# Performance work log

Measured on AMD Instinct MI355X. Metric: run time of the kernel, lower is better.

The kernel has to match this reference:

```python
import jax, jax.numpy as jnp
import numpy as np

HASH = 1 << 12
EPS = 1e-5
_OFFS = [(dx, dy, dz) for dx in (-1, 0, 1) for dy in (-1, 0, 1) for dz in (-1, 0, 1)]
_KOFF = [k for k, o in enumerate(_OFFS) if o != (0, 0, 0)]  # 26 non-center taps
_CENTER = 13


def _hkey(c):
    c = c.astype(np.int64)
    return (c[:, 0] * HASH + c[:, 1]) * HASH + c[:, 2]


def _rand_coords(rng, n, R):
    idx = rng.choice(R ** 3, size=n, replace=False)
    return np.stack(np.unravel_index(idx, (R, R, R)), axis=1).astype(np.int64)


def _conv3_maps(coords):
    # ME kernel map for a 3x3x3 stride-1 conv (in coords == out coords):
    # per non-center tap, (gather_idx, scatter_idx) pairs found by hash lookup.
    n = coords.shape[0]
    keys = _hkey(coords)
    order = np.argsort(keys)
    skeys = keys[order]
    ins, outs = [], []
    for k in _KOFF:
        qk = _hkey(coords + np.asarray(_OFFS[k], np.int64))
        pos = np.clip(np.searchsorted(skeys, qk), 0, n - 1)
        valid = skeys[pos] == qk
        outs.append(np.nonzero(valid)[0].astype(np.int32))
        ins.append(order[pos[valid]].astype(np.int32))
    m = max(len(a) for a in ins)
    im = np.zeros((26, m), np.int32)    # pad gathers with row 0
    om = np.full((26, m), n, np.int32)  # pad scatters into scrap row n (dropped)
    for j in range(26):
        im[j, :len(ins[j])] = ins[j]
        om[j, :len(outs[j])] = outs[j]
    return np.stack([im, om])  # [2, 26, M]


def _children(coords):
    # generative transpose conv k=2 s=2 output coords, ordered o*n + i
    offs = np.array([[a, b, c] for a in (0, 1) for b in (0, 1) for c in (0, 1)], np.int64)
    return (2 * coords[None] + offs[:, None]).reshape(-1, 3)


def _union(ca, cb):
    # sparse-tensor addition domain: union of coordinate sets
    ka, kb = _hkey(ca), _hkey(cb)
    ku = np.unique(np.concatenate([ka, kb]))
    cu = np.stack([ku // (HASH * HASH), (ku // HASH) % HASH, ku % HASH], axis=1)
    return cu, np.searchsorted(ku, ka).astype(np.int32), np.searchsorted(ku, kb).astype(np.int32)


def _sconv3(x, W, m):
    # sparse 3^3 conv as gather-GEMM-scatter; center tap is a plain GEMM
    n = x.shape[0]
    acc = jnp.zeros((n + 1, W.shape[2]), x.dtype)
    for j, k in enumerate(_KOFF):
        acc = acc.at[m[1, j]].add(x[m[0, j]] @ W[k])
    return acc[:n] + x @ W[_CENTER]


def _bn_elu(x, p):
    # MinkowskiBatchNorm (training-mode batch stats over active voxels) + ELU
    mu = jnp.mean(x, axis=0)
    var = jnp.mean(jnp.square(x - mu), axis=0)
    return jax.nn.elu(p[0] * (x - mu) * jax.lax.rsqrt(var + EPS) + p[1])


def _up_block(x, Wt, Wc, m, pa, pb):
    # generative transpose conv (every voxel emits 8 children, order o*n+i) -> BN -> ELU -> conv3 -> BN -> ELU
    t = jnp.einsum('nc,ocd->ond', x, Wt).reshape(-1, Wt.shape[2])
    return _bn_elu(_sconv3(_bn_elu(t, pa), Wc, m), pb)


def setup_inputs() -> dict:
    rng = np.random.default_rng(0)
    N2, N1, N0 = 1200, 6000, 16000
    C2 = _rand_coords(rng, N2, 40)
    C1 = _rand_coords(rng, N1, 80)
    C0 = _rand_coords(rng, N0, 160)
    G2 = _children(C2)                       # coords after up_block_2 transpose conv
    U1, lat1_idx, up1_idx = _union(C1, G2)   # inputs[1] + x domain
    G1 = _children(U1)
    U0, lat0_idx, up0_idx = _union(C0, G1)   # inputs[0] + x domain

    key = jax.random.key(0)
    ks = list(jax.random.split(key, 32))
    kit = iter(ks)

    def w(shape, fan_in):
        return jax.random.normal(next(kit), shape, jnp.float32) * np.float32(1.0 / np.sqrt(fan_in))

    def bn(c):
        g = 1.0 + 0.1 * jax.random.normal(next(kit), (c,), jnp.float32)
        b = 0.1 * jax.random.normal(next(kit), (c,), jnp.float32)
        return jnp.stack([g, b])

    return dict(
        feats0=jax.random.normal(next(kit), (N0, 64), jnp.float32),
        feats1=jax.random.normal(next(kit), (N1, 128), jnp.float32),
        feats2=jax.random.normal(next(kit), (N2, 256), jnp.float32),
        w_out0=w((27, 64, 128), 27 * 64),
        w_out1=w((27, 128, 128), 27 * 128),
        w_out2=w((27, 256, 128), 27 * 256),
        wt2=w((8, 256, 128), 256),
        wu2=w((27, 128, 128), 27 * 128),
        wt1=w((8, 128, 64), 128),
        wu1=w((27, 64, 64), 27 * 64),
        bn_out0=bn(128), bn_out1=bn(128), bn_out2=bn(128),
        bn_up2a=bn(128), bn_up2b=bn(128),
        bn_up1a=bn(64), bn_up1b=bn(64),
        u1_base=jnp.zeros((U1.shape[0], 128), jnp.float32),
        u0_base=jnp.zeros((U0.shape[0], 64), jnp.float32),
        m_c2=jnp.asarray(_conv3_maps(C2)),
        m_g2=jnp.asarray(_conv3_maps(G2)),
        m_u1=jnp.asarray(_conv3_maps(U1)),
        m_g1=jnp.asarray(_conv3_maps(G1)),
        m_u0=jnp.asarray(_conv3_maps(U0)),
        lat1_idx=jnp.asarray(lat1_idx), up1_idx=jnp.asarray(up1_idx),
        lat0_idx=jnp.asarray(lat0_idx), up0_idx=jnp.asarray(up0_idx),
    )


def reference(feats0, feats1, feats2, w_out0, w_out1, w_out2, wt2, wu2, wt1, wu1,
              bn_out0, bn_out1, bn_out2, bn_up2a, bn_up2b, bn_up1a, bn_up1b,
              u1_base, u0_base, m_c2, m_g2, m_u1, m_g1, m_u0,
              lat1_idx, up1_idx, lat0_idx, up0_idx):
    # i = 2 (top)
    out2 = _bn_elu(_sconv3(feats2, w_out2, m_c2), bn_out2)
    t = _up_block(feats2, wt2, wu2, m_g2, bn_up2a, bn_up2b)
    # i = 1: sparse add over union of coords, then out/up blocks
    x1 = u1_base.at[lat1_idx].add(feats1).at[up1_idx].add(t)
    out1 = _bn_elu(_sconv3(x1, w_out1, m_u1), bn_out1)
    t = _up_block(x1, wt1, wu1, m_g1, bn_up1a, bn_up1b)
    # i = 0
    x0 = u0_base.at[lat0_idx].add(feats0).at[up0_idx].add(t)
    out0 = _bn_elu(_sconv3(x0, w_out0, m_u0), bn_out0)
    return out0, out1, out2
```

## Files before the change

### kernel.cpp

```cpp
#include <hip/hip_runtime.h>

typedef __bf16 bf16x8 __attribute__((ext_vector_type(8)));
typedef float  f32x4  __attribute__((ext_vector_type(4)));
typedef unsigned short u16x8 __attribute__((ext_vector_type(8)));

__device__ __forceinline__ float b2f(unsigned short u) {
    union { unsigned int i; float f; } v; v.i = ((unsigned int)u) << 16; return v.f;
}
__device__ __forceinline__ unsigned short f2b(float f) {
    union { float f; unsigned int i; } v; v.f = f;
    unsigned int u = v.i;
    return (unsigned short)((u + 0x7fffu + ((u >> 16) & 1u)) >> 16);
}

__global__ void table_init(int* __restrict__ tab, int n)
{
    int idx = blockIdx.x * blockDim.x + threadIdx.x;
    if (idx >= n * 27) return;
    tab[idx] = ((idx % 27) == 13) ? (idx / 27) : n;
}

__global__ void table_fill(int* __restrict__ tab, const int* __restrict__ map, int M, int n)
{
    int tid = blockIdx.x * blockDim.x + threadIdx.x;
    if (tid >= 26 * M) return;
    int j = tid / M, q = tid - j * M;
    int om = map[(26 + j) * M + q];
    if (om < n) {
        int k = (j < 13) ? j : j + 1;
        tab[om * 27 + k] = map[j * M + q];
    }
}

__global__ void pack_w(const float* __restrict__ W, unsigned short* __restrict__ P,
                       int total, int log2Cout, int log2KC)
{
    int tid = blockIdx.x * blockDim.x + threadIdx.x;
    if (tid >= total) return;
    int jj   = tid & 7;
    int cout = (tid >> 3) & ((1 << log2Cout) - 1);
    int rest = tid >> (3 + log2Cout);
    int quad = rest & 3;
    int kj   = rest >> 2;
    int kc   = kj & ((1 << log2KC) - 1);
    int j    = kj >> log2KC;
    int Cin  = (1 << log2KC) * 32;
    int Cout = 1 << log2Cout;
    P[tid] = f2b(W[((size_t)j * Cin + kc * 32 + quad * 8 + jj) * Cout + cout]);
}

__global__ void cast_bf16(const float* __restrict__ X, unsigned short* __restrict__ Y, int nElem)
{
    int tid = blockIdx.x * blockDim.x + threadIdx.x;
    if (tid < nElem) Y[tid] = f2b(X[tid]);
}

template<int T, int KC, int RT, bool OUTBF16>
__global__ __launch_bounds__(256) void conv_mfma_st(
    const unsigned short* __restrict__ Xb, const unsigned short* __restrict__ P,
    const int* __restrict__ tab, void* __restrict__ OutV, float* __restrict__ St,
    int n, int nblk)
{
    constexpr int Cin = KC * 32, Cout = 64 * T;
    constexpr int ROWS = RT * 16;
    constexpr int STRIDE = KC * 32 + 8;
    constexpr int CHUNKS = KC * 4;
    constexpr int RPR = 256 / CHUNKS;
    constexpr int NRD = ROWS / RPR;
    __shared__ int tps[ROWS * 27];
    __shared__ unsigned short abuf[2][ROWS * STRIDE];

    const int t = threadIdx.x, lane = t & 63, wv = t >> 6;
    const int m = lane & 15, quad = lane >> 4;

    const int q = nblk >> 3, rr = nblk & 7;
    const int xcd = blockIdx.x & 7, pos = blockIdx.x >> 3;
    const int bswz = (xcd < rr) ? (xcd * (q + 1) + pos) : (rr * (q + 1) + (xcd - rr) * q + pos);
    const int r0 = bswz * ROWS;
    int rows = n - r0; if (rows > ROWS) rows = ROWS;

    for (int e = t; e < ROWS * 27; e += 256)
        tps[e] = (e < rows * 27) ? tab[(size_t)r0 * 27 + e] : n;
    __syncthreads();

    const int sr = t / CHUNKS;
    const int sc = t % CHUNKS;

    f32x4 acc[RT][T];
    #pragma unroll
    for (int rt = 0; rt < RT; rt++)
        #pragma unroll
        for (int c = 0; c < T; c++) acc[rt][c] = f32x4{0.f, 0.f, 0.f, 0.f};

    uint4 sreg[NRD];

    #pragma unroll
    for (int rd = 0; rd < NRD; rd++) {
        int r = rd * RPR + sr;
        int in = tps[r * 27];
        sreg[rd] = *reinterpret_cast<const uint4*>(Xb + (size_t)in * Cin + sc * 8);
    }
    #pragma unroll
    for (int rd = 0; rd < NRD; rd++) {
        int r = rd * RPR + sr;
        *reinterpret_cast<uint4*>(&abuf[0][r * STRIDE + sc * 8]) = sreg[rd];
    }
    __syncthreads();

    for (int j = 0; j < 27; j++) {
        const int cur = j & 1;
        if (j + 1 < 27) {
            #pragma unroll
            for (int rd = 0; rd < NRD; rd++) {
                int r = rd * RPR + sr;
                int in = tps[r * 27 + j + 1];
                sreg[rd] = *reinterpret_cast<const uint4*>(Xb + (size_t)in * Cin + sc * 8);
            }
        }
        #pragma unroll
        for (int kc = 0; kc < KC; kc++) {
            bf16x8 a[RT];
            #pragma unroll
            for (int rt = 0; rt < RT; rt++)
                a[rt] = *reinterpret_cast<const bf16x8*>(&abuf[cur][(rt * 16 + m) * STRIDE + kc * 32 + quad * 8]);
            const unsigned short* bp = P + ((size_t)((j * KC + kc) * 4 + quad) * Cout + wv * (T * 16)) * 8;
            #pragma unroll
            for (int c = 0; c < T; c++) {
                bf16x8 b = *reinterpret_cast<const bf16x8*>(bp + (c * 16 + m) * 8);
                #pragma unroll
                for (int rt = 0; rt < RT; rt++)
                    acc[rt][c] = __builtin_amdgcn_mfma_f32_16x16x32_bf16(a[rt], b, acc[rt][c], 0, 0, 0);
            }
        }
        if (j + 1 < 27) {
            #pragma unroll
            for (int rd = 0; rd < NRD; rd++) {
                int r = rd * RPR + sr;
                *reinterpret_cast<uint4*>(&abuf[cur ^ 1][r * STRIDE + sc * 8]) = sreg[rd];
            }
        }
        __syncthreads();
    }

    #pragma unroll
    for (int c = 0; c < T; c++) {
        const int cout = (wv * T + c) * 16 + m;
        float s = 0.f, ss = 0.f;
        #pragma unroll
        for (int rt = 0; rt < RT; rt++) {
            #pragma unroll
            for (int reg = 0; reg < 4; reg++) {
                int r = rt * 16 + quad * 4 + reg;
                if (r < rows) {
                    float v = acc[rt][c][reg];
                    size_t off = (size_t)(r0 + r) * Cout + cout;
                    if (OUTBF16) {
                        unsigned short h = f2b(v);
                        ((unsigned short*)OutV)[off] = h;
                        v = b2f(h);
                    } else {
                        ((float*)OutV)[off] = v;
                    }
                    s += v; ss += v * v;
                }
            }
        }
        if (St) {
            s  += __shfl_xor(s, 16);  ss += __shfl_xor(ss, 16);
            s  += __shfl_xor(s, 32);  ss += __shfl_xor(ss, 32);
            if (quad == 0) {
                float* Sr = St + (size_t)(blockIdx.x & 7) * 2 * Cout;
                atomicAdd(&Sr[cout], s);
                atomicAdd(&Sr[Cout + cout], ss);
            }
        }
    }
}

template<int T, int RB, bool OUTBF16>
__global__ __launch_bounds__(256) void conv_mfma(
    const unsigned short* __restrict__ Xb, const unsigned short* __restrict__ P,
    const int* __restrict__ tab, void* __restrict__ OutV, int n, int Cin, int KC, int nblk)
{
    const int Cout = 64 * T;
    const int ROWS = RB * 16;
    __shared__ int tps[RB * 16 * 27];
    __shared__ int vld[27];
    const int t = threadIdx.x, lane = t & 63, wv = t >> 6;
    const int m = lane & 15, quad = lane >> 4;

    const int q = nblk >> 3, rr = nblk & 7;
    const int xcd = blockIdx.x & 7, pos = blockIdx.x >> 3;
    const int bswz = (xcd < rr) ? (xcd * (q + 1) + pos) : (rr * (q + 1) + (xcd - rr) * q + pos);
    const int r0 = bswz * ROWS;
    int rows = n - r0; if (rows > ROWS) rows = ROWS;

    for (int e = t; e < ROWS * 27; e += 256)
        tps[e] = (e < rows * 27) ? tab[(size_t)r0 * 27 + e] : n;
    __syncthreads();
    if constexpr (RB == 1) {
        if (t < 27) {
            int v = 0;
            for (int r = 0; r < 16; r++) v |= (tps[r * 27 + t] < n) ? 1 : 0;
            vld[t] = v;
        }
        __syncthreads();
    }

    f32x4 acc[RB][T];
    #pragma unroll
    for (int rt = 0; rt < RB; rt++)
        #pragma unroll
        for (int c = 0; c < T; c++) acc[rt][c] = f32x4{0.f, 0.f, 0.f, 0.f};

    const unsigned short* Xq = Xb + quad * 8;
    const unsigned short* Pq = P + ((size_t)quad * Cout + wv * (T * 16)) * 8;

    for (int j = 0; j < 27; j++) {
        if constexpr (RB == 1) {
            if (!vld[j]) continue;
        }
        int in[RB];
        #pragma unroll
        for (int rt = 0; rt < RB; rt++) in[rt] = tps[(rt * 16 + m) * 27 + j];
        for (int kc = 0; kc < KC; kc++) {
            bf16x8 a[RB];
            #pragma unroll
            for (int rt = 0; rt < RB; rt++)
                a[rt] = *reinterpret_cast<const bf16x8*>(Xq + (size_t)in[rt] * Cin + kc * 32);
            const unsigned short* bp = Pq + (size_t)((j * KC + kc) * 4) * Cout * 8;
            #pragma unroll
            for (int c = 0; c < T; c++) {
                bf16x8 b = *reinterpret_cast<const bf16x8*>(bp + (c * 16 + m) * 8);
                #pragma unroll
                for (int rt = 0; rt < RB; rt++)
                    acc[rt][c] = __builtin_amdgcn_mfma_f32_16x16x32_bf16(a[rt], b, acc[rt][c], 0, 0, 0);
            }
        }
    }

    #pragma unroll
    for (int c = 0; c < T; c++) {
        int cout = (wv * T + c) * 16 + m;
        #pragma unroll
        for (int rt = 0; rt < RB; rt++) {
            #pragma unroll
            for (int reg = 0; reg < 4; reg++) {
                int r = rt * 16 + quad * 4 + reg;
                if (r < rows) {
                    size_t off = (size_t)(r0 + r) * Cout + cout;
                    if (OUTBF16) ((unsigned short*)OutV)[off] = f2b(acc[rt][c][reg]);
                    else         ((float*)OutV)[off] = acc[rt][c][reg];
                }
            }
        }
    }
}

template<int KC, int T>
__global__ __launch_bounds__(256) void tconv_mfma(
    const unsigned short* __restrict__ Xb, const unsigned short* __restrict__ P,
    unsigned short* __restrict__ Out, int n)
{
    const int Cin = KC * 32, Cout = 64 * T;
    const int t = threadIdx.x, lane = t & 63, wv = t >> 6;
    const int m = lane & 15, quad = lane >> 4;
    const int r0 = blockIdx.x * 16;
    int rows = n - r0; if (rows > 16) rows = 16;

    bf16x8 a[KC];
    #pragma unroll
    for (int kc = 0; kc < KC; kc++) {
        a[kc] = bf16x8{};
        if (m < rows)
            a[kc] = *reinterpret_cast<const bf16x8*>(Xb + (size_t)(r0 + m) * Cin + kc * 32 + quad * 8);
    }

    for (int o = 0; o < 8; o++) {
        f32x4 acc[T];
        #pragma unroll
        for (int c = 0; c < T; c++) acc[c] = f32x4{0.f, 0.f, 0.f, 0.f};
        #pragma unroll
        for (int kc = 0; kc < KC; kc++) {
            const unsigned short* bp = P + ((size_t)((o * KC + kc) * 4 + quad) * Cout + wv * (T * 16)) * 8;
            #pragma unroll
            for (int c = 0; c < T; c++) {
                bf16x8 b = *reinterpret_cast<const bf16x8*>(bp + (c * 16 + m) * 8);
                acc[c] = __builtin_amdgcn_mfma_f32_16x16x32_bf16(a[kc], b, acc[c], 0, 0, 0);
            }
        }
        #pragma unroll
        for (int c = 0; c < T; c++) {
            int cout = (wv * T + c) * 16 + m;
            #pragma unroll
            for (int reg = 0; reg < 4; reg++) {
                int r = quad * 4 + reg;
                if (r < rows)
                    Out[((size_t)o * n + r0 + r) * Cout + cout] = f2b(acc[c][reg]);
            }
        }
    }
}

__global__ void scatter_add_f32(float* __restrict__ dst, const float* __restrict__ src,
                                const int* __restrict__ idx, long total, int C)
{
    long tid = (long)blockIdx.x * blockDim.x + threadIdx.x;
    if (tid >= total) return;
    long r = tid / C;
    int  c = (int)(tid - r * C);
    dst[(long)idx[r] * C + c] += src[tid];
}

__global__ void scatter_add_b16(float* __restrict__ dst, const unsigned short* __restrict__ src,
                                const int* __restrict__ idx, long total, int C)
{
    long tid = (long)blockIdx.x * blockDim.x + threadIdx.x;
    if (tid >= total) return;
    long r = tid / C;
    int  c = (int)(tid - r * C);
    dst[(long)idx[r] * C + c] += b2f(src[tid]);
}

template<bool BF16>
__global__ void bn_stats_k(const void* __restrict__ Xv, float* __restrict__ stats,
                           int n, int C, int rowsPerBlock)
{
    const int t = threadIdx.x;
    const int c = t & (C - 1);
    const int sub = t / C;
    const int nsub = 256 / C;
    int r0 = blockIdx.x * rowsPerBlock + sub;
    int r1 = blockIdx.x * rowsPerBlock + rowsPerBlock;
    if (r1 > n) r1 = n;
    float s = 0.f, ss = 0.f;
    for (int r = r0; r < r1; r += nsub) {
        float v = BF16 ? b2f(((const unsigned short*)Xv)[(long)r * C + c])
                       : ((const float*)Xv)[(long)r * C + c];
        s += v; ss += v * v;
    }
    __shared__ float bs[256];
    __shared__ float bq[256];
    bs[t] = s; bq[t] = ss;
    __syncthreads();
    if (sub == 0) {
        for (int k = 1; k < nsub; k++) { s += bs[k * C + c]; ss += bq[k * C + c]; }
        atomicAdd(&stats[c], s);
        atomicAdd(&stats[C + c], ss);
    }
}

__global__ void bn_finalize(const float* __restrict__ stats, const float* __restrict__ gb,
                            float* __restrict__ scsh, int C, float invn, int nrep)
{
    int c = threadIdx.x;
    if (c >= C) return;
    float sm = 0.f, sq = 0.f;
    for (int r = 0; r < nrep; r++) {
        sm += stats[r * 2 * C + c];
        sq += stats[r * 2 * C + C + c];
    }
    float mu  = sm * invn;
    float var = sq * invn - mu * mu;
    float sc  = gb[c] * rsqrtf(var + 1e-5f);
    scsh[c]     = sc;
    scsh[C + c] = gb[C + c] - mu * sc;
}

__global__ void bn_apply_f32v(float* __restrict__ X, const float* __restrict__ scsh,
                              long total4, int C)
{
    long tid = (long)blockIdx.x * blockDim.x + threadIdx.x;
    if (tid >= total4) return;
    int c0 = (int)((tid * 4) & (C - 1));
    float4 x  = reinterpret_cast<float4*>(X)[tid];
    float4 sc = *reinterpret_cast<const float4*>(&scsh[c0]);
    float4 sh = *reinterpret_cast<const float4*>(&scsh[C + c0]);
    float v0 = x.x * sc.x + sh.x; v0 = (v0 > 0.f) ? v0 : expm1f(v0);
    float v1 = x.y * sc.y + sh.y; v1 = (v1 > 0.f) ? v1 : expm1f(v1);
    float v2 = x.z * sc.z + sh.z; v2 = (v2 > 0.f) ? v2 : expm1f(v2);
    float v3 = x.w * sc.w + sh.w; v3 = (v3 > 0.f) ? v3 : expm1f(v3);
    reinterpret_cast<float4*>(X)[tid] = float4{v0, v1, v2, v3};
}

__global__ void bn_apply_b16v(unsigned short* __restrict__ X, const float* __restrict__ scsh,
                              long total8, int C)
{
    long tid = (long)blockIdx.x * blockDim.x + threadIdx.x;
    if (tid >= total8) return;
    int c0 = (int)((tid * 8) & (C - 1));
    u16x8 x = reinterpret_cast<u16x8*>(X)[tid];
    u16x8 y;
    #pragma unroll
    for (int k = 0; k < 8; k++) {
        float v = b2f(x[k]) * scsh[c0 + k] + scsh[C + c0 + k];
        v = (v > 0.f) ? v : expm1f(v);
        y[k] = f2b(v);
    }
    reinterpret_cast<u16x8*>(X)[tid] = y;
}

extern "C" void kernel_launch(void* const* d_in, const int* in_sizes, int n_in,
                              void* d_out, int out_size, void* d_ws, size_t ws_size,
                              hipStream_t stream)
{
    const float* feats0  = (const float*)d_in[0];
    const float* feats1  = (const float*)d_in[1];
    const float* feats2  = (const float*)d_in[2];
    const float* w_out0  = (const float*)d_in[3];
    const float* w_out1  = (const float*)d_in[4];
    const float* w_out2  = (const float*)d_in[5];
    const float* wt2     = (const float*)d_in[6];
    const float* wu2     = (const float*)d_in[7];
    const float* wt1     = (const float*)d_in[8];
    const float* wu1     = (const float*)d_in[9];
    const float* bn_out0 = (const float*)d_in[10];
    const float* bn_out1 = (const float*)d_in[11];
    const float* bn_out2 = (const float*)d_in[12];
    const float* bn_up2a = (const float*)d_in[13];
    const float* bn_up2b = (const float*)d_in[14];
    const float* bn_up1a = (const float*)d_in[15];
    const float* bn_up1b = (const float*)d_in[16];
    const int* m_c2 = (const int*)d_in[19];
    const int* m_g2 = (const int*)d_in[20];
    const int* m_u1 = (const int*)d_in[21];
    const int* m_g1 = (const int*)d_in[22];
    const int* m_u0 = (const int*)d_in[23];
    const int* lat1 = (const int*)d_in[24];
    const int* up1  = (const int*)d_in[25];
    const int* lat0 = (const int*)d_in[26];
    const int* up0  = (const int*)d_in[27];

    const int N0  = in_sizes[0] / 64;
    const int N1  = in_sizes[1] / 128;
    const int N2  = in_sizes[2] / 256;
    const int U1  = in_sizes[17] / 128;
    const int U0  = in_sizes[18] / 64;
    const int G2n = in_sizes[25];
    const int G1n = in_sizes[27];
    const int Mc2 = in_sizes[19] / 52;
    const int Mg2 = in_sizes[20] / 52;
    const int Mu1 = in_sizes[21] / 52;
    const int Mg1 = in_sizes[22] / 52;
    const int Mu0 = in_sizes[23] / 52;

    float* out0 = (float*)d_out;
    float* out1 = out0 + (size_t)U0 * 128;
    float* out2 = out1 + (size_t)U1 * 128;

    char* wp = (char*)d_ws;
    auto alloc = [&](size_t bytes) -> char* {
        char* r = wp; wp += (bytes + 255) & ~(size_t)255; return r;
    };
    float*          x0   = (float*)alloc((size_t)U0 * 64 * 4);
    unsigned short* t1   = (unsigned short*)alloc((size_t)(G1n + 1) * 64 * 2);
    unsigned short* t1c  = (unsigned short*)alloc((size_t)(G1n + 1) * 64 * 2);
    unsigned short* t2   = (unsigned short*)alloc((size_t)(G2n + 1) * 128 * 2);
    unsigned short* t2c  = (unsigned short*)alloc((size_t)(G2n + 1) * 128 * 2);
    float*          x1   = (float*)alloc((size_t)U1 * 128 * 4);
    unsigned short* x1b  = (unsigned short*)alloc((size_t)(U1 + 1) * 128 * 2);
    unsigned short* x0b  = (unsigned short*)alloc((size_t)(U0 + 1) * 64 * 2);
    unsigned short* f2bb = (unsigned short*)alloc((size_t)(N2 + 1) * 256 * 2);
    unsigned short* pc2  = (unsigned short*)alloc((size_t)27 * 256 * 128 * 2);
    unsigned short* pt2  = (unsigned short*)alloc((size_t)8  * 256 * 128 * 2);
    unsigned short* pg2  = (unsigned short*)alloc((size_t)27 * 128 * 128 * 2);
    unsigned short* pu1  = (unsigned short*)alloc((size_t)27 * 128 * 128 * 2);
    unsigned short* pt1  = (unsigned short*)alloc((size_t)8  * 128 * 64  * 2);
    unsigned short* pg1  = (unsigned short*)alloc((size_t)27 * 64  * 64  * 2);
    unsigned short* pu0  = (unsigned short*)alloc((size_t)27 * 64  * 128 * 2);
    int maxSmall = (U1 > G2n) ? U1 : G2n;
    int*   smallTab = (int*)alloc((size_t)maxSmall * 27 * 4);
    float* stats    = (float*)alloc(8 * 2 * 128 * 4);
    float* scsh     = (float*)alloc(2 * 128 * 4);
    int* tab_g1 = (int*)x0;
    int* tab_u0 = (int*)t1;

    hipMemsetAsync(f2bb + (size_t)N2  * 256, 0, 256 * 2, stream);
    hipMemsetAsync(t2   + (size_t)G2n * 128, 0, 128 * 2, stream);
    hipMemsetAsync(x1b  + (size_t)U1  * 128, 0, 128 * 2, stream);
    hipMemsetAsync(t1   + (size_t)G1n * 64,  0, 64  * 2, stream);
    hipMemsetAsync(x0b  + (size_t)U0  * 64,  0, 64  * 2, stream);

    auto packW = [&](const float* W, unsigned short* P, int taps, int l2co, int l2kc) {
        int total = taps * ((1 << l2kc) * 32) * (1 << l2co);
        pack_w<<<dim3((total + 255) / 256), dim3(256), 0, stream>>>(W, P, total, l2co, l2kc);
    };
    auto cast = [&](const float* X, unsigned short* Y, long nElem) {
        cast_bf16<<<dim3((int)((nElem + 255) / 256)), dim3(256), 0, stream>>>(X, Y, (int)nElem);
    };
    auto buildTab = [&](int* tab, const int* map, int M, int n) {
        table_init<<<dim3((n * 27 + 255) / 256), dim3(256), 0, stream>>>(tab, n);
        table_fill<<<dim3((26 * M + 255) / 256), dim3(256), 0, stream>>>(tab, map, M, n);
    };
    auto conv = [&](const unsigned short* Xb, const unsigned short* P, const int* tab,
                    void* Out, int n, int Cin, int Cout, bool outbf16, float* st) {
        int KC = Cin / 32;
        if (n >= 12000) {
            if (Cout == 128 && KC == 2) {
                int nblk = (n + 63) / 64;
                dim3 g(nblk), b(256);
                if (outbf16) conv_mfma_st<2, 2, 4, true ><<<g, b, 0, stream>>>(Xb, P, tab, Out, st, n, nblk);
                else         conv_mfma_st<2, 2, 4, false><<<g, b, 0, stream>>>(Xb, P, tab, Out, st, n, nblk);
                return;
            }
            if (Cout == 64 && KC == 2) {
                int nblk = (n + 63) / 64;
                dim3 g(nblk), b(256);
                if (outbf16) conv_mfma_st<1, 2, 4, true ><<<g, b, 0, stream>>>(Xb, P, tab, Out, st, n, nblk);
                else         conv_mfma_st<1, 2, 4, false><<<g, b, 0, stream>>>(Xb, P, tab, Out, st, n, nblk);
                return;
            }
            if (Cout == 128 && KC == 4) {
                int nblk = (n + 31) / 32;
                dim3 g(nblk), b(256);
                if (outbf16) conv_mfma_st<2, 4, 2, true ><<<g, b, 0, stream>>>(Xb, P, tab, Out, st, n, nblk);
                else         conv_mfma_st<2, 4, 2, false><<<g, b, 0, stream>>>(Xb, P, tab, Out, st, n, nblk);
                return;
            }
        }
        int RB = (n >= 12000) ? 2 : 1;
        int nblk = (n + RB * 16 - 1) / (RB * 16);
        dim3 g(nblk), b(256);
        #define CONV_CASE(T_, RB_)                                                                        \
            if (Cout == 64 * T_ && RB == RB_) {                                                           \
                if (outbf16) conv_mfma<T_, RB_, true ><<<g, b, 0, stream>>>(Xb, P, tab, Out, n, Cin, KC, nblk); \
                else         conv_mfma<T_, RB_, false><<<g, b, 0, stream>>>(Xb, P, tab, Out, n, Cin, KC, nblk); \
                return;                                                                                   \
            }
        CONV_CASE(2, 2) CONV_CASE(2, 1)
        CONV_CASE(1, 2) CONV_CASE(1, 1)
        #undef CONV_CASE
    };
    auto bnapply = [&](void* X, const float* gb, int n, int C, bool bf16, int nrep) {
        bn_finalize<<<dim3(1), dim3(C), 0, stream>>>(stats, gb, scsh, C, 1.0f / n, nrep);
        if (bf16) {
            long tot8 = (long)n * C / 8;
            bn_apply_b16v<<<dim3((int)((tot8 + 255) / 256)), dim3(256), 0, stream>>>((unsigned short*)X, scsh, tot8, C);
        } else {
            long tot4 = (long)n * C / 4;
            bn_apply_f32v<<<dim3((int)((tot4 + 255) / 256)), dim3(256), 0, stream>>>((float*)X, scsh, tot4, C);
        }
    };
    auto bnelu = [&](void* X, const float* gb, int n, int C, bool bf16) {
        hipMemsetAsync(stats, 0, 2 * C * sizeof(float), stream);
        const int rpb = 512;
        if (bf16) bn_stats_k<true ><<<dim3((n + rpb - 1) / rpb), dim3(256), 0, stream>>>(X, stats, n, C, rpb);
        else      bn_stats_k<false><<<dim3((n + rpb - 1) / rpb), dim3(256), 0, stream>>>(X, stats, n, C, rpb);
        bnapply(X, gb, n, C, bf16, 1);
    };

    cast(feats2, f2bb, (long)N2 * 256);
    packW(w_out2, pc2, 27, 7, 3);
    packW(wt2,    pt2,  8, 7, 3);
    packW(wu2,    pg2, 27, 7, 2);
    packW(w_out1, pu1, 27, 7, 2);
    packW(wt1,    pt1,  8, 6, 2);
    packW(wu1,    pg1, 27, 6, 1);
    packW(w_out0, pu0, 27, 7, 1);

    buildTab(smallTab, m_c2, Mc2, N2);
    conv(f2bb, pc2, smallTab, out2, N2, 256, 128, false, nullptr);
    bnelu(out2, bn_out2, N2, 128, false);
    tconv_mfma<8, 2><<<dim3((N2 + 15) / 16), dim3(256), 0, stream>>>(f2bb, pt2, t2, N2);
    bnelu(t2, bn_up2a, G2n, 128, true);
    buildTab(smallTab, m_g2, Mg2, G2n);
    conv(t2, pg2, smallTab, t2c, G2n, 128, 128, true, nullptr);
    bnelu(t2c, bn_up2b, G2n, 128, true);

    hipMemsetAsync(x1, 0, (size_t)U1 * 128 * sizeof(float), stream);
    {
        long tot = (long)N1 * 128;
        scatter_add_f32<<<dim3((int)((tot + 255) / 256)), dim3(256), 0, stream>>>(x1, feats1, lat1, tot, 128);
        tot = (long)G2n * 128;
        scatter_add_b16<<<dim3((int)((tot + 255) / 256)), dim3(256), 0, stream>>>(x1, t2c, up1, tot, 128);
    }
    cast(x1, x1b, (long)U1 * 128);
    buildTab(smallTab, m_u1, Mu1, U1);
    hipMemsetAsync(stats, 0, 8 * 2 * 128 * sizeof(float), stream);
    conv(x1b, pu1, smallTab, out1, U1, 128, 128, false, stats);
    bnapply(out1, bn_out1, U1, 128, false, 8);
    tconv_mfma<4, 1><<<dim3((U1 + 15) / 16), dim3(256), 0, stream>>>(x1b, pt1, t1, U1);
    bnelu(t1, bn_up1a, G1n, 64, true);
    buildTab(tab_g1, m_g1, Mg1, G1n);
    hipMemsetAsync(stats, 0, 8 * 2 * 64 * sizeof(float), stream);
    conv(t1, pg1, tab_g1, t1c, G1n, 64, 64, true, stats);
    bnapply(t1c, bn_up1b, G1n, 64, true, 8);

    hipMemsetAsync(x0, 0, (size_t)U0 * 64 * sizeof(float), stream);
    {
        long tot = (long)N0 * 64;
        scatter_add_f32<<<dim3((int)((tot + 255) / 256)), dim3(256), 0, stream>>>(x0, feats0, lat0, tot, 64);
        tot = (long)G1n * 64;
        scatter_add_b16<<<dim3((int)((tot + 255) / 256)), dim3(256), 0, stream>>>(x0, t1c, up0, tot, 64);
    }
    buildTab(tab_u0, m_u0, Mu0, U0);
    cast(x0, x0b, (long)U0 * 64);
    hipMemsetAsync(stats, 0, 8 * 2 * 128 * sizeof(float), stream);
    conv(x0b, pu0, tab_u0, out0, U0, 64, 128, false, stats);
    bnapply(out0, bn_out0, U0, 128, false, 8);
}
```

Baseline: 950.1 us.

## Fuse BN+ELU into scatter-add, vectorize cast/scatter kernels, enlarge conv row tile

```diff
diff --git a/kernel.cpp b/kernel.cpp
--- a/kernel.cpp
+++ b/kernel.cpp
@@ -49,10 +49,13 @@
     P[tid] = f2b(W[((size_t)j * Cin + kc * 32 + quad * 8 + jj) * Cout + cout]);
 }
 
-__global__ void cast_bf16(const float* __restrict__ X, unsigned short* __restrict__ Y, int nElem)
-{
-    int tid = blockIdx.x * blockDim.x + threadIdx.x;
-    if (tid < nElem) Y[tid] = f2b(X[tid]);
+__global__ void cast_bf16v(const float* __restrict__ X, unsigned short* __restrict__ Y, long total4)
+{
+    long tid = (long)blockIdx.x * blockDim.x + threadIdx.x;
+    if (tid >= total4) return;
+    float4 x = reinterpret_cast<const float4*>(X)[tid];
+    ushort4 y{f2b(x.x), f2b(x.y), f2b(x.z), f2b(x.w)};
+    reinterpret_cast<ushort4*>(Y)[tid] = y;
 }
 
 template<int T, int KC, int RT, bool OUTBF16>
@@ -302,24 +305,40 @@
     }
 }
 
-__global__ void scatter_add_f32(float* __restrict__ dst, const float* __restrict__ src,
-                                const int* __restrict__ idx, long total, int C)
+__global__ void scatter_set_f32v(float* __restrict__ dst, const float* __restrict__ src,
+                                 const int* __restrict__ idx, long total4, int C4)
 {
     long tid = (long)blockIdx.x * blockDim.x + threadIdx.x;
-    if (tid >= total) return;
-    long r = tid / C;
-    int  c = (int)(tid - r * C);
-    dst[(long)idx[r] * C + c] += src[tid];
-}
-
-__global__ void scatter_add_b16(float* __restrict__ dst, const unsigned short* __restrict__ src,
-                                const int* __restrict__ idx, long total, int C)
+    if (tid >= total4) return;
+    long r = tid / C4;
+    int  c4 = (int)(tid - r * C4);
+    float4 s = reinterpret_cast<const float4*>(src)[tid];
+    reinterpret_cast<float4*>(dst + (long)idx[r] * C4 * 4)[c4] = s;
+}
+
+__global__ void scatter_bn_add_b16v(float* __restrict__ dst, const unsigned short* __restrict__ src,
+                                    const int* __restrict__ idx, const float* __restrict__ scsh,
+                                    long total8, int C)
 {
     long tid = (long)blockIdx.x * blockDim.x + threadIdx.x;
-    if (tid >= total) return;
-    long r = tid / C;
-    int  c = (int)(tid - r * C);
-    dst[(long)idx[r] * C + c] += b2f(src[tid]);
+    if (tid >= total8) return;
+    int C8 = C >> 3;
+    long r = tid / C8;
+    int  c0 = (int)(tid - r * C8) * 8;
+    u16x8 x = reinterpret_cast<const u16x8*>(src)[tid];
+    float* d = dst + (long)idx[r] * C + c0;
+    float4 d0 = *reinterpret_cast<float4*>(d);
+    float4 d1 = *reinterpret_cast<float4*>(d + 4);
+    float v[8];
+    #pragma unroll
+    for (int k = 0; k < 8; k++) {
+        float w = b2f(x[k]) * scsh[c0 + k] + scsh[C + c0 + k];
+        v[k] = (w > 0.f) ? w : expm1f(w);
+    }
+    d0.x += v[0]; d0.y += v[1]; d0.z += v[2]; d0.w += v[3];
+    d1.x += v[4]; d1.y += v[5]; d1.z += v[6]; d1.w += v[7];
+    *reinterpret_cast<float4*>(d)     = d0;
+    *reinterpret_cast<float4*>(d + 4) = d1;
 }
 
 template<bool BF16>
@@ -486,7 +505,8 @@
         pack_w<<<dim3((total + 255) / 256), dim3(256), 0, stream>>>(W, P, total, l2co, l2kc);
     };
     auto cast = [&](const float* X, unsigned short* Y, long nElem) {
-        cast_bf16<<<dim3((int)((nElem + 255) / 256)), dim3(256), 0, stream>>>(X, Y, (int)nElem);
+        long tot4 = nElem / 4;
+        cast_bf16v<<<dim3((int)((tot4 + 255) / 256)), dim3(256), 0, stream>>>(X, Y, tot4);
     };
     auto buildTab = [&](int* tab, const int* map, int M, int n) {
         table_init<<<dim3((n * 27 + 255) / 256), dim3(256), 0, stream>>>(tab, n);
@@ -504,10 +524,10 @@
                 return;
             }
             if (Cout == 64 && KC == 2) {
-                int nblk = (n + 63) / 64;
+                int nblk = (n + 127) / 128;
                 dim3 g(nblk), b(256);
-                if (outbf16) conv_mfma_st<1, 2, 4, true ><<<g, b, 0, stream>>>(Xb, P, tab, Out, st, n, nblk);
-                else         conv_mfma_st<1, 2, 4, false><<<g, b, 0, stream>>>(Xb, P, tab, Out, st, n, nblk);
+                if (outbf16) conv_mfma_st<1, 2, 8, true ><<<g, b, 0, stream>>>(Xb, P, tab, Out, st, n, nblk);
+                else         conv_mfma_st<1, 2, 8, false><<<g, b, 0, stream>>>(Xb, P, tab, Out, st, n, nblk);
                 return;
             }
             if (Cout == 128 && KC == 4) {
@@ -565,14 +585,16 @@
     bnelu(t2, bn_up2a, G2n, 128, true);
     buildTab(smallTab, m_g2, Mg2, G2n);
     conv(t2, pg2, smallTab, t2c, G2n, 128, 128, true, nullptr);
-    bnelu(t2c, bn_up2b, G2n, 128, true);
+    hipMemsetAsync(stats, 0, 2 * 128 * sizeof(float), stream);
+    bn_stats_k<true><<<dim3((G2n + 511) / 512), dim3(256), 0, stream>>>(t2c, stats, G2n, 128, 512);
+    bn_finalize<<<dim3(1), dim3(128), 0, stream>>>(stats, bn_up2b, scsh, 128, 1.0f / G2n, 1);
 
     hipMemsetAsync(x1, 0, (size_t)U1 * 128 * sizeof(float), stream);
     {
-        long tot = (long)N1 * 128;
-        scatter_add_f32<<<dim3((int)((tot + 255) / 256)), dim3(256), 0, stream>>>(x1, feats1, lat1, tot, 128);
-        tot = (long)G2n * 128;
-        scatter_add_b16<<<dim3((int)((tot + 255) / 256)), dim3(256), 0, stream>>>(x1, t2c, up1, tot, 128);
+        long tot4 = (long)N1 * 128 / 4;
+        scatter_set_f32v<<<dim3((int)((tot4 + 255) / 256)), dim3(256), 0, stream>>>(x1, feats1, lat1, tot4, 32);
+        long tot8 = (long)G2n * 128 / 8;
+        scatter_bn_add_b16v<<<dim3((int)((tot8 + 255) / 256)), dim3(256), 0, stream>>>(x1, t2c, up1, scsh, tot8, 128);
     }
     cast(x1, x1b, (long)U1 * 128);
     buildTab(smallTab, m_u1, Mu1, U1);
@@ -584,14 +606,14 @@
     buildTab(tab_g1, m_g1, Mg1, G1n);
     hipMemsetAsync(stats, 0, 8 * 2 * 64 * sizeof(float), stream);
     conv(t1, pg1, tab_g1, t1c, G1n, 64, 64, true, stats);
-    bnapply(t1c, bn_up1b, G1n, 64, true, 8);
+    bn_finalize<<<dim3(1), dim3(64), 0, stream>>>(stats, bn_up1b, scsh, 64, 1.0f / G1n, 8);
 
     hipMemsetAsync(x0, 0, (size_t)U0 * 64 * sizeof(float), stream);
     {
-        long tot = (long)N0 * 64;
-        scatter_add_f32<<<dim3((int)((tot + 255) / 256)), dim3(256), 0, stream>>>(x0, feats0, lat0, tot, 64);
-        tot = (long)G1n * 64;
-        scatter_add_b16<<<dim3((int)((tot + 255) / 256)), dim3(256), 0, stream>>>(x0, t1c, up0, tot, 64);
+        long tot4 = (long)N0 * 64 / 4;
+        scatter_set_f32v<<<dim3((int)((tot4 + 255) / 256)), dim3(256), 0, stream>>>(x0, feats0, lat0, tot4, 16);
+        long tot8 = (long)G1n * 64 / 8;
+        scatter_bn_add_b16v<<<dim3((int)((tot8 + 255) / 256)), dim3(256), 0, stream>>>(x0, t1c, up0, scsh, tot8, 64);
     }
     buildTab(tab_u0, m_u0, Mu0, U0);
     cast(x0, x0b, (long)U0 * 64);
```

Result: faster. 922.6 us (-2.9%).
